# Performance work log

Hardware: AMD Instinct MI355X
Metric: run time of the kernel (lower is better)

Reference implementation:

```python
import jax, jax.numpy as jnp
import numpy as np


def setup_inputs() -> dict:
    key = jax.random.key(0)
    k1, k2, k3, k4 = jax.random.split(key, 4)
    B, N, D, P = 1, 8192, 128, 2  # batch must be 1 (see .view(B,N,N) in source)
    x = jax.random.normal(k1, (B, N, D), dtype=jnp.float32)
    points = jax.random.normal(k2, (B, N, P), dtype=jnp.float32)
    # nn.Linear params, stored as (in, out) so y = x @ W + b
    W1 = jax.random.normal(k3, (2 * D, 2 * D), dtype=jnp.float32) * 0.04
    b1 = jnp.zeros((2 * D,), dtype=jnp.float32)
    W2 = jax.random.normal(k4, (2 * D, D), dtype=jnp.float32) * 0.04
    b2 = jnp.zeros((D,), dtype=jnp.float32)
    return {"x": x, "points": points, "W1": W1, "b1": b1, "W2": W2, "b2": b2, "K": 16}


def reference(x, points, W1, b1, W2, b2, K):
    B, N, _ = points.shape
    D = x.shape[-1]
    # torch.cdist on flattened (B*N, P) points, reshaped to (B, N, N)
    # (valid only for B == 1, matching the original module). Squared distance
    # is monotone in Euclidean distance, so top-k indices are identical.
    pf = points.reshape(B * N, -1)
    sq = jnp.sum(pf * pf, axis=-1)
    d2 = sq[:, None] + sq[None, :] - 2.0 * (pf @ pf.T)  # (BN, BN)
    d2 = d2.reshape(B, N, N)
    # topk(-dist, K+1) -> nearest K+1 (self first), drop self
    _, idx = jax.lax.top_k(-d2, K + 1)  # (B, N, K+1)
    idx = idx[:, :, 1:]  # (B, N, K)
    # gather neighbor features: knn_fts[b, n, k] = x[b, idx[b, n, k]]
    knn = x[jnp.arange(B)[:, None, None], idx]  # (B, N, K, D)
    center = jnp.broadcast_to(x[:, :, None, :], (B, N, K, D))
    local = jnp.concatenate([knn - center, center], axis=-1)  # (B, N, K, 2D)
    h = jax.nn.gelu(local @ W1 + b1, approximate=False)
    h = jax.nn.gelu(h @ W2 + b2, approximate=False)
    return jnp.mean(h, axis=2)  # (B, N, D)
```

## Files before the change

kernel.cpp:

```cpp
#include <hip/hip_runtime.h>

typedef __attribute__((ext_vector_type(8))) short short8;
typedef __attribute__((ext_vector_type(4))) float f32x4;

__device__ __forceinline__ unsigned short f2bf(float f) {
    unsigned int u = __float_as_uint(f);
    unsigned int r = u + 0x7fffu + ((u >> 16) & 1u);
    return (unsigned short)(r >> 16);
}

__device__ __forceinline__ float bf2f(short s) {
    return __uint_as_float(((unsigned int)(unsigned short)s) << 16);
}

__device__ __forceinline__ float gelu_fast(float v) {
    float x2 = v * v;
    float s  = v * fmaf(-0.102943195f, x2, -2.3022077f);
    float e  = __builtin_amdgcn_exp2f(s);
    return v * __builtin_amdgcn_rcpf(1.0f + e);
}

__device__ __forceinline__ unsigned int d2key(float d2) {
    unsigned int u = __float_as_uint(d2);
    return u ^ (((unsigned int)(((int)u) >> 31)) | 0x80000000u);
}

#define U64MAX 0xFFFFFFFFFFFFFFFFull

#define D2_FROM(px, py)                                                          \
    ({ const float sqj_ = __fadd_rn(__fmul_rn((px), (px)), __fmul_rn((py), (py))); \
       const float t_   = fmaf(yi, (py), __fmul_rn(xi, (px)));                     \
       const float s_   = __fadd_rn(sqi, sqj_);                                    \
       fmaf(-2.0f, t_, s_); })

__device__ __forceinline__ unsigned long long bitonic64(unsigned long long v, int lane) {
#pragma unroll
    for (int k = 2; k <= 64; k <<= 1) {
#pragma unroll
        for (int j = k >> 1; j > 0; j >>= 1) {
            unsigned long long pv = __shfl_xor(v, j, 64);
            const bool up  = ((lane & k) == 0);
            const bool low = ((lane & j) == 0);
            const unsigned long long mn = (v < pv) ? v : pv;
            const unsigned long long mx = (v < pv) ? pv : v;
            v = (up == low) ? mn : mx;
        }
    }
    return v;
}

__global__ __launch_bounds__(256) void knn_kernel(
        const float* __restrict__ points,
        const float* __restrict__ W1, const float* __restrict__ W2,
        unsigned short* __restrict__ W1t, unsigned short* __restrict__ W2t,
        int* __restrict__ idx_out) {
    __shared__ unsigned long long cand[4][128];
    __shared__ int ccnt[4];

    const int bid = blockIdx.x;
    const int tid = threadIdx.x;

    if (bid < 384) {
        int g = bid * 256 + tid;
        if (g < 65536) {
            int d = g >> 8, c = g & 255;
            W1t[c * 256 + d] = f2bf(W1[g]);
        } else if (g < 98304) {
            int g2 = g - 65536;
            int d = g2 >> 7, c = g2 & 127;
            W2t[c * 256 + d] = f2bf(W2[g2]);
        }
        return;
    }

    const int wv   = tid >> 6;
    const int lane = tid & 63;
    const int q    = ((bid - 384) << 2) + wv;

    const float xi = points[q * 2 + 0];
    const float yi = points[q * 2 + 1];
    const float sqi = __fadd_rn(__fmul_rn(xi, xi), __fmul_rn(yi, yi));

    const float4* p4 = (const float4*)points;

    unsigned long long vmin = U64MAX;
#pragma unroll 8
    for (int j = 0; j < 64; ++j) {
        const float4 pp = p4[j * 64 + lane];
        const int i0 = j * 128 + lane * 2;
        {
            const float d2 = D2_FROM(pp.x, pp.y);
            unsigned long long pk = ((unsigned long long)d2key(d2) << 32) | (unsigned int)i0;
            vmin = (pk < vmin) ? pk : vmin;
        }
        {
            const float d2 = D2_FROM(pp.z, pp.w);
            unsigned long long pk = ((unsigned long long)d2key(d2) << 32) | (unsigned int)(i0 + 1);
            vmin = (pk < vmin) ? pk : vmin;
        }
    }

    unsigned long long v = bitonic64(vmin, lane);
    const unsigned long long T64 = __shfl(v, 16, 64);
    const unsigned int Tkey = (unsigned int)(T64 >> 32);

    unsigned long long* candw = cand[wv];
    int* ccntw = &ccnt[wv];
    if (lane == 0) *ccntw = 0;
    __syncthreads();

#pragma unroll 4
    for (int j = 0; j < 64; ++j) {
        const float4 pp = p4[j * 64 + lane];
        const int i0 = j * 128 + lane * 2;
        {
            const float d2 = D2_FROM(pp.x, pp.y);
            const unsigned int key = d2key(d2);
            if (key <= Tkey) {
                int pos = atomicAdd(ccntw, 1);
                if (pos < 128)
                    candw[pos] = ((unsigned long long)key << 32) | (unsigned int)i0;
            }
        }
        {
            const float d2 = D2_FROM(pp.z, pp.w);
            const unsigned int key = d2key(d2);
            if (key <= Tkey) {
                int pos = atomicAdd(ccntw, 1);
                if (pos < 128)
                    candw[pos] = ((unsigned long long)key << 32) | (unsigned int)(i0 + 1);
            }
        }
    }
    __syncthreads();

    const int n = *ccntw < 128 ? *ccntw : 128;
    if (n <= 64) {
        unsigned long long v0 = (lane < n) ? candw[lane] : U64MAX;
        v0 = bitonic64(v0, lane);
        if (lane >= 1 && lane <= 16)
            idx_out[q * 16 + lane - 1] = (int)(unsigned int)(v0 & 0xFFFFFFFFull);
    } else {
        unsigned long long v0 = (lane < n)      ? candw[lane]      : U64MAX;
        unsigned long long v1 = (lane + 64 < n) ? candw[lane + 64] : U64MAX;
#pragma unroll 1
        for (int pick = 0; pick < 17; ++pick) {
            unsigned long long m = (v0 < v1) ? v0 : v1;
#pragma unroll
            for (int d = 1; d < 64; d <<= 1) {
                unsigned long long pm = __shfl_xor(m, d, 64);
                m = (pm < m) ? pm : m;
            }
            if (pick > 0 && lane == 0)
                idx_out[q * 16 + pick - 1] = (int)(unsigned int)(m & 0xFFFFFFFFull);
            if (v0 == m) v0 = U64MAX;
            else if (v1 == m) v1 = U64MAX;
        }
    }
}

__global__ __launch_bounds__(256) void gemmAD_kernel(
        const float* __restrict__ x, const unsigned short* __restrict__ W1t,
        const float* __restrict__ b1,
        unsigned short* __restrict__ Abf, unsigned short* __restrict__ Dbf) {
    __shared__ unsigned short sx[64 * 136];
    const int tid = threadIdx.x;
    const int rb  = (blockIdx.x >> 1) * 64;
    const int cb  = (blockIdx.x & 1) * 128;

    {
        const int r   = ((tid >> 6) << 4) | (tid & 15);
        const int seg = (tid >> 4) & 3;
        const float* xr = x + (rb + r) * 128 + seg * 32;
        unsigned short* dst = sx + r * 136 + seg * 32;
#pragma unroll
        for (int u = 0; u < 8; ++u) {
            float4 a = ((const float4*)xr)[u];
            uint2 w;
            w.x = (unsigned)f2bf(a.x) | ((unsigned)f2bf(a.y) << 16);
            w.y = (unsigned)f2bf(a.z) | ((unsigned)f2bf(a.w) << 16);
            *(uint2*)(dst + u * 4) = w;
        }
    }
    __syncthreads();

    const int lane = tid & 63, wv = tid >> 6;
    const int m = lane & 15, quad = lane >> 4;
    const int ko0 = quad * 8;

    f32x4 accA[8], accC[8];
#pragma unroll
    for (int i = 0; i < 8; ++i) { accA[i] = (f32x4){0,0,0,0}; accC[i] = (f32x4){0,0,0,0}; }

#pragma unroll
    for (int ks = 0; ks < 4; ++ks) {
        const int ko = ks * 32 + ko0;
        short8 af[4], bA[2], bC[2];
#pragma unroll
        for (int rt = 0; rt < 4; ++rt)
            af[rt] = *(const short8*)(sx + (rt * 16 + m) * 136 + ko);
#pragma unroll
        for (int ct = 0; ct < 2; ++ct) {
            const unsigned short* wp = W1t + (cb + wv * 32 + ct * 16 + m) * 256 + ko;
            bA[ct] = *(const short8*)(wp);
            bC[ct] = *(const short8*)(wp + 128);
        }
#pragma unroll
        for (int rt = 0; rt < 4; ++rt)
#pragma unroll
            for (int ct = 0; ct < 2; ++ct) {
                accA[rt * 2 + ct] = __builtin_amdgcn_mfma_f32_16x16x32_bf16(
                    af[rt], bA[ct], accA[rt * 2 + ct], 0, 0, 0);
                accC[rt * 2 + ct] = __builtin_amdgcn_mfma_f32_16x16x32_bf16(
                    af[rt], bC[ct], accC[rt * 2 + ct], 0, 0, 0);
            }
    }

#pragma unroll
    for (int ct = 0; ct < 2; ++ct) {
        const int col = cb + wv * 32 + ct * 16 + m;
        const float bias = b1[col];
#pragma unroll
        for (int rt = 0; rt < 4; ++rt)
#pragma unroll
            for (int j = 0; j < 4; ++j) {
                const int row = rb + rt * 16 + quad * 4 + j;
                float a = accA[rt * 2 + ct][j];
                float d = accC[rt * 2 + ct][j] - a + bias;
                Abf[row * 256 + col] = f2bf(a);
                Dbf[row * 256 + col] = f2bf(d);
            }
    }
}

__global__ __launch_bounds__(256) void mlp_kernel(
        const unsigned short* __restrict__ Abf, const unsigned short* __restrict__ Dbf,
        const unsigned short* __restrict__ W2t, const float* __restrict__ b2,
        const int* __restrict__ idx, float* __restrict__ out) {
    __shared__ unsigned short sh[64 * 264];
    const int tid = threadIdx.x;
    const int qb  = blockIdx.x << 2;

    {
        const int r   = ((tid >> 6) << 4) | (tid & 15);
        const int seg = (tid >> 4) & 3;
        const int gq  = qb + (r >> 4);
        const int nb  = idx[(gq << 4) + (r & 15)];
        const unsigned short* arow = Abf + nb * 256 + seg * 64;
        const unsigned short* drow = Dbf + gq * 256 + seg * 64;
        unsigned short* dst = sh + r * 264 + seg * 64;
#pragma unroll
        for (int u = 0; u < 8; ++u) {
            short8 av = *(const short8*)(arow + u * 8);
            short8 dv = *(const short8*)(drow + u * 8);
            short8 hv;
#pragma unroll
            for (int e = 0; e < 8; ++e) {
                float h = bf2f(av[e]) + bf2f(dv[e]);
                hv[e] = (short)f2bf(gelu_fast(h));
            }
            *(short8*)(dst + u * 8) = hv;
        }
    }
    __syncthreads();

    const int lane = tid & 63, wv = tid >> 6;
    const int m = lane & 15, quad = lane >> 4;
    const int ko0 = quad * 8;

    f32x4 acc2[8];
#pragma unroll
    for (int i = 0; i < 8; ++i) acc2[i] = (f32x4){0.f, 0.f, 0.f, 0.f};
#pragma unroll
    for (int ks = 0; ks < 8; ++ks) {
        const int ko = ks * 32 + ko0;
        short8 af[4], bfr[2];
#pragma unroll
        for (int rt = 0; rt < 4; ++rt)
            af[rt] = *(const short8*)(sh + (rt * 16 + m) * 264 + ko);
#pragma unroll
        for (int ct = 0; ct < 2; ++ct)
            bfr[ct] = *(const short8*)(W2t + (wv * 32 + ct * 16 + m) * 256 + ko);
#pragma unroll
        for (int rt = 0; rt < 4; ++rt)
#pragma unroll
            for (int ct = 0; ct < 2; ++ct)
                acc2[rt * 2 + ct] = __builtin_amdgcn_mfma_f32_16x16x32_bf16(
                    af[rt], bfr[ct], acc2[rt * 2 + ct], 0, 0, 0);
    }

#pragma unroll
    for (int ct = 0; ct < 2; ++ct) {
        const int col = wv * 32 + ct * 16 + m;
        const float bias = b2[col];
#pragma unroll
        for (int rt = 0; rt < 4; ++rt) {
            float s = 0.f;
#pragma unroll
            for (int j = 0; j < 4; ++j)
                s += gelu_fast(acc2[rt * 2 + ct][j] + bias);
            s += __shfl_xor(s, 16, 64);
            s += __shfl_xor(s, 32, 64);
            if (quad == 0) out[(qb + rt) * 128 + col] = s * 0.0625f;
        }
    }
}

extern "C" void kernel_launch(void* const* d_in, const int* in_sizes, int n_in,
                              void* d_out, int out_size, void* d_ws, size_t ws_size,
                              hipStream_t stream) {
    const float* x      = (const float*)d_in[0];
    const float* points = (const float*)d_in[1];
    const float* W1     = (const float*)d_in[2];
    const float* b1     = (const float*)d_in[3];
    const float* W2     = (const float*)d_in[4];
    const float* b2     = (const float*)d_in[5];
    float* out = (float*)d_out;

    char* ws = (char*)d_ws;
    unsigned short* W1t = (unsigned short*)ws;
    unsigned short* W2t = (unsigned short*)(ws + 131072);
    int*            idx = (int*)(ws + 196608);
    unsigned short* Abf = (unsigned short*)(ws + 720896);
    unsigned short* Dbf = (unsigned short*)(ws + 4915200);

    knn_kernel<<<2432, 256, 0, stream>>>(points, W1, W2, W1t, W2t, idx);
    gemmAD_kernel<<<256, 256, 0, stream>>>(x, W1t, b1, Abf, Dbf);
    mlp_kernel<<<2048, 256, 0, stream>>>(Abf, Dbf, W2t, b2, idx, out);
}
```

Baseline: 151.4 us.

## Process four queries per wave in kNN with float prefilter and slack threshold

Each wave now handles four query points, so every loaded point tile is reused across four queries instead of one, and the block count drops to match. The threshold pass uses a cheaper float distance (norm plus -2x·p via FMAs) with a float bitonic sort and a small slack. Candidates are then re-keyed with the exact rounding-matched distance. This trades extra registers and LDS plus a heuristic slack margin for fewer global loads and less ALU work per query; the slack could overflow the 128-candidate buffer or change tie behaviour.

```diff
diff --git a/kernel.cpp b/kernel.cpp
--- a/kernel.cpp
+++ b/kernel.cpp
@@ -27,10 +27,10 @@
 
 #define U64MAX 0xFFFFFFFFFFFFFFFFull
 
-#define D2_FROM(px, py)                                                          \
+#define D2_FROM_Q(px, py, XI, YI, SQI)                                           \
     ({ const float sqj_ = __fadd_rn(__fmul_rn((px), (px)), __fmul_rn((py), (py))); \
-       const float t_   = fmaf(yi, (py), __fmul_rn(xi, (px)));                     \
-       const float s_   = __fadd_rn(sqi, sqj_);                                    \
+       const float t_   = fmaf((YI), (py), __fmul_rn((XI), (px)));                 \
+       const float s_   = __fadd_rn((SQI), sqj_);                                  \
        fmaf(-2.0f, t_, s_); })
 
 __device__ __forceinline__ unsigned long long bitonic64(unsigned long long v, int lane) {
@@ -49,13 +49,41 @@
     return v;
 }
 
+__device__ __forceinline__ float bitonic64f(float v, int lane) {
+#pragma unroll
+    for (int k = 2; k <= 64; k <<= 1) {
+#pragma unroll
+        for (int j = k >> 1; j > 0; j >>= 1) {
+            float pv = __shfl_xor(v, j, 64);
+            const bool up  = ((lane & k) == 0);
+            const bool low = ((lane & j) == 0);
+            const float mn = fminf(v, pv);
+            const float mx = fmaxf(v, pv);
+            v = (up == low) ? mn : mx;
+        }
+    }
+    return v;
+}
+
+__device__ __forceinline__ void insert_cand(
+        unsigned long long* crow, int* cnt,
+        float px, float py, float XI, float YI, float SQI, int i) {
+    const float d2 = D2_FROM_Q(px, py, XI, YI, SQI);
+    const unsigned int key = d2key(d2);
+    int pos = atomicAdd(cnt, 1);
+    if (pos < 128)
+        crow[pos] = ((unsigned long long)key << 32) | (unsigned int)i;
+}
+
+#define KNN_SLACK 2.0e-3f
+
 __global__ __launch_bounds__(256) void knn_kernel(
         const float* __restrict__ points,
         const float* __restrict__ W1, const float* __restrict__ W2,
         unsigned short* __restrict__ W1t, unsigned short* __restrict__ W2t,
         int* __restrict__ idx_out) {
-    __shared__ unsigned long long cand[4][128];
-    __shared__ int ccnt[4];
+    __shared__ unsigned long long cand[16][128];
+    __shared__ int ccnt[16];
 
     const int bid = blockIdx.x;
     const int tid = threadIdx.x;
@@ -73,88 +101,94 @@
         return;
     }
 
-    const int wv   = tid >> 6;
-    const int lane = tid & 63;
-    const int q    = ((bid - 384) << 2) + wv;
-
-    const float xi = points[q * 2 + 0];
-    const float yi = points[q * 2 + 1];
-    const float sqi = __fadd_rn(__fmul_rn(xi, xi), __fmul_rn(yi, yi));
+    const int wv    = tid >> 6;
+    const int lane  = tid & 63;
+    const int qbase = ((bid - 384) << 4) | (wv << 2);
+
+    float xi[4], yi[4], sqi_[4], n2x[4], n2y[4];
+#pragma unroll
+    for (int t = 0; t < 4; ++t) {
+        xi[t] = points[(qbase + t) * 2 + 0];
+        yi[t] = points[(qbase + t) * 2 + 1];
+        sqi_[t] = __fadd_rn(__fmul_rn(xi[t], xi[t]), __fmul_rn(yi[t], yi[t]));
+        n2x[t] = -2.0f * xi[t];
+        n2y[t] = -2.0f * yi[t];
+    }
 
     const float4* p4 = (const float4*)points;
 
-    unsigned long long vmin = U64MAX;
+    if (lane < 4) ccnt[(wv << 2) + lane] = 0;
+
+    float vmn[4] = {1e30f, 1e30f, 1e30f, 1e30f};
 #pragma unroll 8
     for (int j = 0; j < 64; ++j) {
         const float4 pp = p4[j * 64 + lane];
-        const int i0 = j * 128 + lane * 2;
-        {
-            const float d2 = D2_FROM(pp.x, pp.y);
-            unsigned long long pk = ((unsigned long long)d2key(d2) << 32) | (unsigned int)i0;
-            vmin = (pk < vmin) ? pk : vmin;
-        }
-        {
-            const float d2 = D2_FROM(pp.z, pp.w);
-            unsigned long long pk = ((unsigned long long)d2key(d2) << 32) | (unsigned int)(i0 + 1);
-            vmin = (pk < vmin) ? pk : vmin;
-        }
-    }
-
-    unsigned long long v = bitonic64(vmin, lane);
-    const unsigned long long T64 = __shfl(v, 16, 64);
-    const unsigned int Tkey = (unsigned int)(T64 >> 32);
-
-    unsigned long long* candw = cand[wv];
-    int* ccntw = &ccnt[wv];
-    if (lane == 0) *ccntw = 0;
+        const float sqa = fmaf(pp.x, pp.x, pp.y * pp.y);
+        const float sqb = fmaf(pp.z, pp.z, pp.w * pp.w);
+#pragma unroll
+        for (int t = 0; t < 4; ++t) {
+            const float da = fmaf(n2x[t], pp.x, fmaf(n2y[t], pp.y, sqa));
+            const float db = fmaf(n2x[t], pp.z, fmaf(n2y[t], pp.w, sqb));
+            vmn[t] = fminf(fminf(da, db), vmn[t]);
+        }
+    }
+
+    float Ta[4];
+#pragma unroll
+    for (int t = 0; t < 4; ++t) {
+        const float s = bitonic64f(vmn[t], lane);
+        Ta[t] = __shfl(s, 16, 64) + KNN_SLACK;
+    }
+
     __syncthreads();
 
 #pragma unroll 4
     for (int j = 0; j < 64; ++j) {
         const float4 pp = p4[j * 64 + lane];
         const int i0 = j * 128 + lane * 2;
-        {
-            const float d2 = D2_FROM(pp.x, pp.y);
-            const unsigned int key = d2key(d2);
-            if (key <= Tkey) {
-                int pos = atomicAdd(ccntw, 1);
-                if (pos < 128)
-                    candw[pos] = ((unsigned long long)key << 32) | (unsigned int)i0;
+        const float sqa = fmaf(pp.x, pp.x, pp.y * pp.y);
+        const float sqb = fmaf(pp.z, pp.z, pp.w * pp.w);
+#pragma unroll
+        for (int t = 0; t < 4; ++t) {
+            const float da = fmaf(n2x[t], pp.x, fmaf(n2y[t], pp.y, sqa));
+            const float db = fmaf(n2x[t], pp.z, fmaf(n2y[t], pp.w, sqb));
+            if (da <= Ta[t])
+                insert_cand(cand[(wv << 2) + t], &ccnt[(wv << 2) + t],
+                            pp.x, pp.y, xi[t], yi[t], sqi_[t], i0);
+            if (db <= Ta[t])
+                insert_cand(cand[(wv << 2) + t], &ccnt[(wv << 2) + t],
+                            pp.z, pp.w, xi[t], yi[t], sqi_[t], i0 + 1);
+        }
+    }
+    __syncthreads();
+
+#pragma unroll 1
+    for (int qi = 0; qi < 4; ++qi) {
+        const int q = qbase + qi;
+        unsigned long long* candw = cand[(wv << 2) + qi];
+        const int cc = ccnt[(wv << 2) + qi];
+        const int n = cc < 128 ? cc : 128;
+        if (n <= 64) {
+            unsigned long long v0 = (lane < n) ? candw[lane] : U64MAX;
+            v0 = bitonic64(v0, lane);
+            if (lane >= 1 && lane <= 16)
+                idx_out[q * 16 + lane - 1] = (int)(unsigned int)(v0 & 0xFFFFFFFFull);
+        } else {
+            unsigned long long v0 = (lane < n)      ? candw[lane]      : U64MAX;
+            unsigned long long v1 = (lane + 64 < n) ? candw[lane + 64] : U64MAX;
+#pragma unroll 1
+            for (int pick = 0; pick < 17; ++pick) {
+                unsigned long long m = (v0 < v1) ? v0 : v1;
+#pragma unroll
+                for (int d = 1; d < 64; d <<= 1) {
+                    unsigned long long pm = __shfl_xor(m, d, 64);
+                    m = (pm < m) ? pm : m;
+                }
+                if (pick > 0 && lane == 0)
+                    idx_out[q * 16 + pick - 1] = (int)(unsigned int)(m & 0xFFFFFFFFull);
+                if (v0 == m) v0 = U64MAX;
+                else if (v1 == m) v1 = U64MAX;
             }
-        }
-        {
-            const float d2 = D2_FROM(pp.z, pp.w);
-            const unsigned int key = d2key(d2);
-            if (key <= Tkey) {
-                int pos = atomicAdd(ccntw, 1);
-                if (pos < 128)
-                    candw[pos] = ((unsigned long long)key << 32) | (unsigned int)(i0 + 1);
-            }
-        }
-    }
-    __syncthreads();
-
-    const int n = *ccntw < 128 ? *ccntw : 128;
-    if (n <= 64) {
-        unsigned long long v0 = (lane < n) ? candw[lane] : U64MAX;
-        v0 = bitonic64(v0, lane);
-        if (lane >= 1 && lane <= 16)
-            idx_out[q * 16 + lane - 1] = (int)(unsigned int)(v0 & 0xFFFFFFFFull);
-    } else {
-        unsigned long long v0 = (lane < n)      ? candw[lane]      : U64MAX;
-        unsigned long long v1 = (lane + 64 < n) ? candw[lane + 64] : U64MAX;
-#pragma unroll 1
-        for (int pick = 0; pick < 17; ++pick) {
-            unsigned long long m = (v0 < v1) ? v0 : v1;
-#pragma unroll
-            for (int d = 1; d < 64; d <<= 1) {
-                unsigned long long pm = __shfl_xor(m, d, 64);
-                m = (pm < m) ? pm : m;
-            }
-            if (pick > 0 && lane == 0)
-                idx_out[q * 16 + pick - 1] = (int)(unsigned int)(m & 0xFFFFFFFFull);
-            if (v0 == m) v0 = U64MAX;
-            else if (v1 == m) v1 = U64MAX;
         }
     }
 }
@@ -324,7 +358,7 @@
     unsigned short* Abf = (unsigned short*)(ws + 720896);
     unsigned short* Dbf = (unsigned short*)(ws + 4915200);
 
-    knn_kernel<<<2432, 256, 0, stream>>>(points, W1, W2, W1t, W2t, idx);
+    knn_kernel<<<896, 256, 0, stream>>>(points, W1, W2, W1t, W2t, idx);
     gemmAD_kernel<<<256, 256, 0, stream>>>(x, W1t, b1, Abf, Dbf);
     mlp_kernel<<<2048, 256, 0, stream>>>(Abf, Dbf, W2t, b2, idx, out);
 }
```

Result: no change. 149.8 us (-1.1%).
